# Kernel optimization log

Measured on AMD Instinct MI355X. Metric: run time of the kernel, lower is better.

## Reference

```python
import jax, jax.numpy as jnp
import numpy as np

NEG_SLOPE = 0.01  # torch nn.LeakyReLU default


def setup_inputs() -> dict:
    key = jax.random.key(0)
    k1, k2, k3, k4 = jax.random.split(key, 4)
    N, D = 8192, 64
    x = jax.random.normal(k1, (N, D), dtype=jnp.float32)
    W = jax.random.normal(k2, (D, D), dtype=jnp.float32) * (1.0 / np.sqrt(D))
    b = jax.random.normal(k3, (D,), dtype=jnp.float32) * 0.01
    a = jax.random.normal(k4, (2 * D, 1), dtype=jnp.float32)
    return {"x": x, "W": W, "b": b, "a": a}


def reference(x, W, b, a):
    # h = Linear(x): torch stores weight as [out, in], y = x @ W.T + b
    h = x @ W.T + b  # [N, D]
    D = h.shape[1]
    a1 = a[:D, 0]   # weights on the column node (e_x[i,j] = x_j)
    a2 = a[D:, 0]   # weights on the row node    (e_y[i,j] = x_i)
    s1 = h @ a1     # [N], contribution of node j
    s2 = h @ a2     # [N], contribution of node i
    # score[i, j] = a1.h_j + a2.h_i  (equivalent to expand+concat+matmul)
    scores = s2[:, None] + s1[None, :]                       # [N, N]
    scores = jnp.where(scores >= 0, scores, NEG_SLOPE * scores)  # leaky_relu
    att = jax.nn.softmax(scores, axis=1)                     # softmax over j
    # NOTE: forward multiplies attention with the ORIGINAL x, not h
    return att @ x                                           # [N, D]
```

## Files before the change

kernel.cpp:

```cpp
#include <hip/hip_runtime.h>

#define NEG_SLOPE 0.01f
#define LOG2E 1.4426950408889634f

constexpr int N = 8192;
constexpr int D = 64;
constexpr int PB = 32;
constexpr int RB = 32;
constexpr int NW = 8;

typedef __bf16 bf16x8 __attribute__((ext_vector_type(8)));
typedef float f32x4 __attribute__((ext_vector_type(4)));

#if __has_builtin(__builtin_amdgcn_exp2f)
#define EXP2(x) __builtin_amdgcn_exp2f(x)
#else
#define EXP2(x) exp2f(x)
#endif

__global__ __launch_bounds__(256) void gat_prep(
    const float* __restrict__ x, const float* __restrict__ W_,
    const float* __restrict__ b, const float* __restrict__ a,
    float* __restrict__ s1g, float* __restrict__ s2g,
    float* __restrict__ blockmax, bf16x8* __restrict__ xf) {
  __shared__ float w1s[D], w2s[D], cs[2];
  __shared__ float s1loc[PB];

  const int t = threadIdx.x;
  const int bid = blockIdx.x;

  if (t < 128) {
    const int sel = t >> 6, d = t & 63;
    const float* av = a + sel * D;
    float acc = 0.f;
#pragma unroll
    for (int k = 0; k < D; ++k) acc += W_[k * D + d] * av[k];
    (sel ? w2s : w1s)[d] = acc * LOG2E;
  }
  if (t == 128 || t == 129) {
    const int sel = t - 128;
    float acc = 0.f;
    for (int d = 0; d < D; ++d) acc += b[d] * a[sel * D + d];
    cs[sel] = acc * LOG2E;
  }
  __syncthreads();

  {
    const int r = t >> 3, seg = t & 7;
    const int gi = bid * PB + r;
    const float4 xa = *(const float4*)(x + (size_t)gi * D + seg * 8);
    const float4 xb = *(const float4*)(x + (size_t)gi * D + seg * 8 + 4);
    float p1 = xa.x * w1s[seg * 8 + 0] + xa.y * w1s[seg * 8 + 1] +
               xa.z * w1s[seg * 8 + 2] + xa.w * w1s[seg * 8 + 3] +
               xb.x * w1s[seg * 8 + 4] + xb.y * w1s[seg * 8 + 5] +
               xb.z * w1s[seg * 8 + 6] + xb.w * w1s[seg * 8 + 7];
    float p2 = xa.x * w2s[seg * 8 + 0] + xa.y * w2s[seg * 8 + 1] +
               xa.z * w2s[seg * 8 + 2] + xa.w * w2s[seg * 8 + 3] +
               xb.x * w2s[seg * 8 + 4] + xb.y * w2s[seg * 8 + 5] +
               xb.z * w2s[seg * 8 + 6] + xb.w * w2s[seg * 8 + 7];
#pragma unroll
    for (int off = 4; off; off >>= 1) {
      p1 += __shfl_xor(p1, off, 64);
      p2 += __shfl_xor(p2, off, 64);
    }
    if (seg == 0) {
      const float v1 = p1 + cs[0], v2 = p2 + cs[1];
      s1g[gi] = v1;
      s2g[gi] = v2;
      s1loc[r] = v1;
    }
  }

  {
    const int dt = t >> 6, fl = t & 63;
    const int jb = bid * PB + ((fl >> 4) << 3);
    const int col = dt * 16 + (fl & 15);
    bf16x8 f;
#pragma unroll
    for (int q = 0; q < 8; ++q) f[q] = (__bf16)x[(size_t)(jb + q) * D + col];
    xf[(bid << 8) | (dt << 6) | fl] = f;
  }
  __syncthreads();
  if (t == 0) {
    float m = s1loc[0];
#pragma unroll
    for (int r = 1; r < PB; ++r) m = fmaxf(m, s1loc[r]);
    blockmax[bid] = m;
  }
}

__global__ __launch_bounds__(512, 2) void gat_main(
    const bf16x8* __restrict__ xf, const float* __restrict__ s1g,
    const float* __restrict__ s2g, const float* __restrict__ blockmax,
    float* __restrict__ out) {
  __shared__ float s1s[N];
  __shared__ float accT[NW][RB][65];
  __shared__ float zt[NW][RB];
  __shared__ float gms;

  const int t = threadIdx.x;
  const int lane = t & 63;
  const int w = t >> 6;
  const int arow = lane & 15;
  const int grp = lane >> 4;
  const int ibase = blockIdx.x * RB;

#pragma unroll
  for (int k = 0; k < N / 4 / 512; ++k)
    ((float4*)s1s)[k * 512 + t] = ((const float4*)s1g)[k * 512 + t];

  if (t < 64) {
    float v = fmaxf(fmaxf(blockmax[lane], blockmax[lane + 64]),
                    fmaxf(blockmax[lane + 128], blockmax[lane + 192]));
#pragma unroll
    for (int off = 32; off; off >>= 1) v = fmaxf(v, __shfl_xor(v, off, 64));
    if (lane == 0) gms = v;
  }
  __syncthreads();
  const float gm = gms;

  const float s2v0 = s2g[ibase + arow];
  const float s2v1 = s2g[ibase + 16 + arow];
  const float tm0 = s2v0 + gm, tm1 = s2v1 + gm;
  const float mneg0 = -fmaxf(tm0, NEG_SLOPE * tm0);
  const float mneg1 = -fmaxf(tm1, NEG_SLOPE * tm1);
  const float A0 = s2v0 + mneg0, B0 = fmaf(NEG_SLOPE, s2v0, mneg0);
  const float A1 = s2v1 + mneg1, B1 = fmaf(NEG_SLOPE, s2v1, mneg1);

  f32x4 a00 = {0.f, 0.f, 0.f, 0.f}, a01 = a00, a02 = a00, a03 = a00;
  f32x4 a10 = a00, a11 = a00, a12 = a00, a13 = a00;
  f32x4 az0 = a00, az1 = a00;
  bf16x8 ones;
#pragma unroll
  for (int q = 0; q < 8; ++q) ones[q] = (__bf16)1.0f;

  bf16x8 pA0, pA1, pA2, pA3, pB0, pB1, pB2, pB3;
  {
    const int fa = w << 8;
    pA0 = xf[fa + 0 * 64 + lane]; pA1 = xf[fa + 1 * 64 + lane];
    pA2 = xf[fa + 2 * 64 + lane]; pA3 = xf[fa + 3 * 64 + lane];
    const int fb = (w + NW) << 8;
    pB0 = xf[fb + 0 * 64 + lane]; pB1 = xf[fb + 1 * 64 + lane];
    pB2 = xf[fb + 2 * 64 + lane]; pB3 = xf[fb + 3 * 64 + lane];
  }

  auto process = [&](const bf16x8& x0, const bf16x8& x1, const bf16x8& x2,
                     const bf16x8& x3, int c) {
    const float4 sa = *(const float4*)&s1s[c * 32 + grp * 8];
    const float4 sb = *(const float4*)&s1s[c * 32 + grp * 8 + 4];
    bf16x8 pa0, pa1;
    const float* sv = &sa.x;
#pragma unroll
    for (int q = 0; q < 4; ++q) {
      const float s = sv[q];
      pa0[q] = (__bf16)EXP2(fmaxf(s + A0, fmaf(NEG_SLOPE, s, B0)));
      pa1[q] = (__bf16)EXP2(fmaxf(s + A1, fmaf(NEG_SLOPE, s, B1)));
    }
    const float* sw = &sb.x;
#pragma unroll
    for (int q = 0; q < 4; ++q) {
      const float s = sw[q];
      pa0[4 + q] = (__bf16)EXP2(fmaxf(s + A0, fmaf(NEG_SLOPE, s, B0)));
      pa1[4 + q] = (__bf16)EXP2(fmaxf(s + A1, fmaf(NEG_SLOPE, s, B1)));
    }
    a00 = __builtin_amdgcn_mfma_f32_16x16x32_bf16(pa0, x0, a00, 0, 0, 0);
    a01 = __builtin_amdgcn_mfma_f32_16x16x32_bf16(pa0, x1, a01, 0, 0, 0);
    a02 = __builtin_amdgcn_mfma_f32_16x16x32_bf16(pa0, x2, a02, 0, 0, 0);
    a03 = __builtin_amdgcn_mfma_f32_16x16x32_bf16(pa0, x3, a03, 0, 0, 0);
    az0 = __builtin_amdgcn_mfma_f32_16x16x32_bf16(pa0, ones, az0, 0, 0, 0);
    a10 = __builtin_amdgcn_mfma_f32_16x16x32_bf16(pa1, x0, a10, 0, 0, 0);
    a11 = __builtin_amdgcn_mfma_f32_16x16x32_bf16(pa1, x1, a11, 0, 0, 0);
    a12 = __builtin_amdgcn_mfma_f32_16x16x32_bf16(pa1, x2, a12, 0, 0, 0);
    a13 = __builtin_amdgcn_mfma_f32_16x16x32_bf16(pa1, x3, a13, 0, 0, 0);
    az1 = __builtin_amdgcn_mfma_f32_16x16x32_bf16(pa1, ones, az1, 0, 0, 0);
  };

  int c0 = w;
  constexpr int PAIRS = N / 32 / NW / 2;
  for (int i = 0; i < PAIRS; ++i) {
    process(pA0, pA1, pA2, pA3, c0);
    {
      const int cn = (i == PAIRS - 1) ? c0 : c0 + 2 * NW;
      const int f = cn << 8;
      pA0 = xf[f + 0 * 64 + lane]; pA1 = xf[f + 1 * 64 + lane];
      pA2 = xf[f + 2 * 64 + lane]; pA3 = xf[f + 3 * 64 + lane];
    }
    process(pB0, pB1, pB2, pB3, c0 + NW);
    {
      const int cn = (i == PAIRS - 1) ? c0 + NW : c0 + 3 * NW;
      const int f = cn << 8;
      pB0 = xf[f + 0 * 64 + lane]; pB1 = xf[f + 1 * 64 + lane];
      pB2 = xf[f + 2 * 64 + lane]; pB3 = xf[f + 3 * 64 + lane];
    }
    c0 += 2 * NW;
  }

  if (arow == 0) {
#pragma unroll
    for (int reg = 0; reg < 4; ++reg) {
      zt[w][grp * 4 + reg] = az0[reg];
      zt[w][16 + grp * 4 + reg] = az1[reg];
    }
  }
#pragma unroll
  for (int reg = 0; reg < 4; ++reg) {
    accT[w][grp * 4 + reg][0 * 16 + arow] = a00[reg];
    accT[w][grp * 4 + reg][1 * 16 + arow] = a01[reg];
    accT[w][grp * 4 + reg][2 * 16 + arow] = a02[reg];
    accT[w][grp * 4 + reg][3 * 16 + arow] = a03[reg];
    accT[w][16 + grp * 4 + reg][0 * 16 + arow] = a10[reg];
    accT[w][16 + grp * 4 + reg][1 * 16 + arow] = a11[reg];
    accT[w][16 + grp * 4 + reg][2 * 16 + arow] = a12[reg];
    accT[w][16 + grp * 4 + reg][3 * 16 + arow] = a13[reg];
  }
  __syncthreads();

#pragma unroll
  for (int k = 0; k < 4; ++k) {
    const int r = w * 4 + k;
    float s = 0.f, z = 0.f;
#pragma unroll
    for (int v = 0; v < NW; ++v) {
      s += accT[v][r][lane];
      z += zt[v][r];
    }
    out[(size_t)(ibase + r) * D + lane] = s / z;
  }
}

extern "C" void kernel_launch(void* const* d_in, const int* in_sizes, int n_in,
                              void* d_out, int out_size, void* d_ws, size_t ws_size,
                              hipStream_t stream) {
  const float* x = (const float*)d_in[0];
  const float* W = (const float*)d_in[1];
  const float* b = (const float*)d_in[2];
  const float* a = (const float*)d_in[3];

  float* s1 = (float*)d_ws;
  float* s2 = s1 + N;
  float* blockmax = s2 + N;
  bf16x8* xf = (bf16x8*)((char*)d_ws + (1u << 20));
  float* out = (float*)d_out;

  gat_prep<<<N / PB, 256, 0, stream>>>(x, W, b, a, s1, s2, blockmax, xf);
  gat_main<<<N / RB, 512, 0, stream>>>(xf, s1, s2, blockmax, out);
}
```

Baseline: 83.75 us.

## Double row tile per block and split the key range into two halves

Each block now handles 64 query rows instead of 32, so every loaded xf fragment feeds twice as many MFMAs. The key dimension is split across two blocks per row tile to keep the block count at 256. The partial numerators and denominators are written to workspace and merged by a new combine kernel. This costs more accumulator registers, an extra kernel launch, and a round trip through global memory for the partial outputs.

Result: no change. 83.29 us (-0.6%).

```diff
diff --git a/kernel.cpp b/kernel.cpp
--- a/kernel.cpp
+++ b/kernel.cpp
@@ -6,8 +6,9 @@
 constexpr int N = 8192;
 constexpr int D = 64;
 constexpr int PB = 32;
-constexpr int RB = 32;
+constexpr int RB = 64;
 constexpr int NW = 8;
+constexpr int NWIN_H = 128;
 
 typedef __bf16 bf16x8 __attribute__((ext_vector_type(8)));
 typedef float f32x4 __attribute__((ext_vector_type(4)));
@@ -92,9 +93,9 @@
 __global__ __launch_bounds__(512, 2) void gat_main(
     const bf16x8* __restrict__ xf, const float* __restrict__ s1g,
     const float* __restrict__ s2g, const float* __restrict__ blockmax,
-    float* __restrict__ out) {
-  __shared__ float s1s[N];
-  __shared__ float accT[NW][RB][65];
+    float* __restrict__ pOut, float* __restrict__ pZ) {
+  __shared__ float s1s[NWIN_H * 32];
+  __shared__ float accT[NW][32][65];
   __shared__ float zt[NW][RB];
   __shared__ float gms;
 
@@ -103,11 +104,14 @@
   const int w = t >> 6;
   const int arow = lane & 15;
   const int grp = lane >> 4;
-  const int ibase = blockIdx.x * RB;
-
-#pragma unroll
-  for (int k = 0; k < N / 4 / 512; ++k)
-    ((float4*)s1s)[k * 512 + t] = ((const float4*)s1g)[k * 512 + t];
+  const int bid = blockIdx.x;
+  const int itile = bid >> 1, half = bid & 1;
+  const int ibase = itile * RB;
+  const int jw0 = half * NWIN_H;
+
+#pragma unroll
+  for (int k = 0; k < 2; ++k)
+    ((float4*)s1s)[k * 512 + t] = ((const float4*)(s1g + jw0 * 32))[k * 512 + t];
 
   if (t < 64) {
     float v = fmaxf(fmaxf(blockmax[lane], blockmax[lane + 64]),
@@ -119,49 +123,64 @@
   __syncthreads();
   const float gm = gms;
 
-  const float s2v0 = s2g[ibase + arow];
-  const float s2v1 = s2g[ibase + 16 + arow];
-  const float tm0 = s2v0 + gm, tm1 = s2v1 + gm;
-  const float mneg0 = -fmaxf(tm0, NEG_SLOPE * tm0);
-  const float mneg1 = -fmaxf(tm1, NEG_SLOPE * tm1);
-  const float A0 = s2v0 + mneg0, B0 = fmaf(NEG_SLOPE, s2v0, mneg0);
-  const float A1 = s2v1 + mneg1, B1 = fmaf(NEG_SLOPE, s2v1, mneg1);
+  float A0v, A1v, A2v, A3v, B0v, B1v, B2v, B3v;
+  {
+    const float s0 = s2g[ibase + 0 * 16 + arow];
+    const float s1v = s2g[ibase + 1 * 16 + arow];
+    const float s2v = s2g[ibase + 2 * 16 + arow];
+    const float s3v = s2g[ibase + 3 * 16 + arow];
+    const float t0 = s0 + gm, t1 = s1v + gm, t2 = s2v + gm, t3 = s3v + gm;
+    const float m0 = -fmaxf(t0, NEG_SLOPE * t0);
+    const float m1 = -fmaxf(t1, NEG_SLOPE * t1);
+    const float m2 = -fmaxf(t2, NEG_SLOPE * t2);
+    const float m3 = -fmaxf(t3, NEG_SLOPE * t3);
+    A0v = s0 + m0;  B0v = fmaf(NEG_SLOPE, s0, m0);
+    A1v = s1v + m1; B1v = fmaf(NEG_SLOPE, s1v, m1);
+    A2v = s2v + m2; B2v = fmaf(NEG_SLOPE, s2v, m2);
+    A3v = s3v + m3; B3v = fmaf(NEG_SLOPE, s3v, m3);
+  }
 
   f32x4 a00 = {0.f, 0.f, 0.f, 0.f}, a01 = a00, a02 = a00, a03 = a00;
   f32x4 a10 = a00, a11 = a00, a12 = a00, a13 = a00;
-  f32x4 az0 = a00, az1 = a00;
+  f32x4 a20 = a00, a21 = a00, a22 = a00, a23 = a00;
+  f32x4 a30 = a00, a31 = a00, a32 = a00, a33 = a00;
+  f32x4 az0 = a00, az1 = a00, az2 = a00, az3 = a00;
   bf16x8 ones;
 #pragma unroll
   for (int q = 0; q < 8; ++q) ones[q] = (__bf16)1.0f;
 
-  bf16x8 pA0, pA1, pA2, pA3, pB0, pB1, pB2, pB3;
+  bf16x8 bA0, bA1, bA2, bA3, bB0, bB1, bB2, bB3;
   {
-    const int fa = w << 8;
-    pA0 = xf[fa + 0 * 64 + lane]; pA1 = xf[fa + 1 * 64 + lane];
-    pA2 = xf[fa + 2 * 64 + lane]; pA3 = xf[fa + 3 * 64 + lane];
-    const int fb = (w + NW) << 8;
-    pB0 = xf[fb + 0 * 64 + lane]; pB1 = xf[fb + 1 * 64 + lane];
-    pB2 = xf[fb + 2 * 64 + lane]; pB3 = xf[fb + 3 * 64 + lane];
+    const int fa = (jw0 + w) << 8;
+    bA0 = xf[fa + 0 * 64 + lane]; bA1 = xf[fa + 1 * 64 + lane];
+    bA2 = xf[fa + 2 * 64 + lane]; bA3 = xf[fa + 3 * 64 + lane];
+    const int fb = (jw0 + w + 8) << 8;
+    bB0 = xf[fb + 0 * 64 + lane]; bB1 = xf[fb + 1 * 64 + lane];
+    bB2 = xf[fb + 2 * 64 + lane]; bB3 = xf[fb + 3 * 64 + lane];
   }
 
   auto process = [&](const bf16x8& x0, const bf16x8& x1, const bf16x8& x2,
-                     const bf16x8& x3, int c) {
-    const float4 sa = *(const float4*)&s1s[c * 32 + grp * 8];
-    const float4 sb = *(const float4*)&s1s[c * 32 + grp * 8 + 4];
-    bf16x8 pa0, pa1;
+                     const bf16x8& x3, int lw) {
+    const float4 sa = *(const float4*)&s1s[lw * 32 + grp * 8];
+    const float4 sb = *(const float4*)&s1s[lw * 32 + grp * 8 + 4];
+    bf16x8 pa0, pa1, pa2, pa3;
     const float* sv = &sa.x;
 #pragma unroll
     for (int q = 0; q < 4; ++q) {
       const float s = sv[q];
-      pa0[q] = (__bf16)EXP2(fmaxf(s + A0, fmaf(NEG_SLOPE, s, B0)));
-      pa1[q] = (__bf16)EXP2(fmaxf(s + A1, fmaf(NEG_SLOPE, s, B1)));
+      pa0[q] = (__bf16)EXP2(fmaxf(s + A0v, fmaf(NEG_SLOPE, s, B0v)));
+      pa1[q] = (__bf16)EXP2(fmaxf(s + A1v, fmaf(NEG_SLOPE, s, B1v)));
+      pa2[q] = (__bf16)EXP2(fmaxf(s + A2v, fmaf(NEG_SLOPE, s, B2v)));
+      pa3[q] = (__bf16)EXP2(fmaxf(s + A3v, fmaf(NEG_SLOPE, s, B3v)));
     }
     const float* sw = &sb.x;
 #pragma unroll
     for (int q = 0; q < 4; ++q) {
       const float s = sw[q];
-      pa0[4 + q] = (__bf16)EXP2(fmaxf(s + A0, fmaf(NEG_SLOPE, s, B0)));
-      pa1[4 + q] = (__bf16)EXP2(fmaxf(s + A1, fmaf(NEG_SLOPE, s, B1)));
+      pa0[4 + q] = (__bf16)EXP2(fmaxf(s + A0v, fmaf(NEG_SLOPE, s, B0v)));
+      pa1[4 + q] = (__bf16)EXP2(fmaxf(s + A1v, fmaf(NEG_SLOPE, s, B1v)));
+      pa2[4 + q] = (__bf16)EXP2(fmaxf(s + A2v, fmaf(NEG_SLOPE, s, B2v)));
+      pa3[4 + q] = (__bf16)EXP2(fmaxf(s + A3v, fmaf(NEG_SLOPE, s, B3v)));
     }
     a00 = __builtin_amdgcn_mfma_f32_16x16x32_bf16(pa0, x0, a00, 0, 0, 0);
     a01 = __builtin_amdgcn_mfma_f32_16x16x32_bf16(pa0, x1, a01, 0, 0, 0);
@@ -173,58 +192,110 @@
     a12 = __builtin_amdgcn_mfma_f32_16x16x32_bf16(pa1, x2, a12, 0, 0, 0);
     a13 = __builtin_amdgcn_mfma_f32_16x16x32_bf16(pa1, x3, a13, 0, 0, 0);
     az1 = __builtin_amdgcn_mfma_f32_16x16x32_bf16(pa1, ones, az1, 0, 0, 0);
+    a20 = __builtin_amdgcn_mfma_f32_16x16x32_bf16(pa2, x0, a20, 0, 0, 0);
+    a21 = __builtin_amdgcn_mfma_f32_16x16x32_bf16(pa2, x1, a21, 0, 0, 0);
+    a22 = __builtin_amdgcn_mfma_f32_16x16x32_bf16(pa2, x2, a22, 0, 0, 0);
+    a23 = __builtin_amdgcn_mfma_f32_16x16x32_bf16(pa2, x3, a23, 0, 0, 0);
+    az2 = __builtin_amdgcn_mfma_f32_16x16x32_bf16(pa2, ones, az2, 0, 0, 0);
+    a30 = __builtin_amdgcn_mfma_f32_16x16x32_bf16(pa3, x0, a30, 0, 0, 0);
+    a31 = __builtin_amdgcn_mfma_f32_16x16x32_bf16(pa3, x1, a31, 0, 0, 0);
+    a32 = __builtin_amdgcn_mfma_f32_16x16x32_bf16(pa3, x2, a32, 0, 0, 0);
+    a33 = __builtin_amdgcn_mfma_f32_16x16x32_bf16(pa3, x3, a33, 0, 0, 0);
+    az3 = __builtin_amdgcn_mfma_f32_16x16x32_bf16(pa3, ones, az3, 0, 0, 0);
   };
 
-  int c0 = w;
-  constexpr int PAIRS = N / 32 / NW / 2;
-  for (int i = 0; i < PAIRS; ++i) {
-    process(pA0, pA1, pA2, pA3, c0);
+  for (int it = 0; it < 8; ++it) {
+    const int lwA = w + 16 * it;
+    process(bA0, bA1, bA2, bA3, lwA);
     {
-      const int cn = (i == PAIRS - 1) ? c0 : c0 + 2 * NW;
-      const int f = cn << 8;
-      pA0 = xf[f + 0 * 64 + lane]; pA1 = xf[f + 1 * 64 + lane];
-      pA2 = xf[f + 2 * 64 + lane]; pA3 = xf[f + 3 * 64 + lane];
-    }
-    process(pB0, pB1, pB2, pB3, c0 + NW);
+      const int lwn = (it == 7) ? lwA : lwA + 16;
+      const int f = (jw0 + lwn) << 8;
+      bA0 = xf[f + 0 * 64 + lane]; bA1 = xf[f + 1 * 64 + lane];
+      bA2 = xf[f + 2 * 64 + lane]; bA3 = xf[f + 3 * 64 + lane];
+    }
+    const int lwB = w + 16 * it + 8;
+    process(bB0, bB1, bB2, bB3, lwB);
     {
-      const int cn = (i == PAIRS - 1) ? c0 + NW : c0 + 3 * NW;
-      const int f = cn << 8;
-      pB0 = xf[f + 0 * 64 + lane]; pB1 = xf[f + 1 * 64 + lane];
-      pB2 = xf[f + 2 * 64 + lane]; pB3 = xf[f + 3 * 64 + lane];
-    }
-    c0 += 2 * NW;
+      const int lwn = (it == 7) ? lwB : lwB + 16;
+      const int f = (jw0 + lwn) << 8;
+      bB0 = xf[f + 0 * 64 + lane]; bB1 = xf[f + 1 * 64 + lane];
+      bB2 = xf[f + 2 * 64 + lane]; bB3 = xf[f + 3 * 64 + lane];
+    }
   }
 
   if (arow == 0) {
 #pragma unroll
     for (int reg = 0; reg < 4; ++reg) {
-      zt[w][grp * 4 + reg] = az0[reg];
-      zt[w][16 + grp * 4 + reg] = az1[reg];
-    }
-  }
-#pragma unroll
-  for (int reg = 0; reg < 4; ++reg) {
-    accT[w][grp * 4 + reg][0 * 16 + arow] = a00[reg];
-    accT[w][grp * 4 + reg][1 * 16 + arow] = a01[reg];
-    accT[w][grp * 4 + reg][2 * 16 + arow] = a02[reg];
-    accT[w][grp * 4 + reg][3 * 16 + arow] = a03[reg];
-    accT[w][16 + grp * 4 + reg][0 * 16 + arow] = a10[reg];
-    accT[w][16 + grp * 4 + reg][1 * 16 + arow] = a11[reg];
-    accT[w][16 + grp * 4 + reg][2 * 16 + arow] = a12[reg];
-    accT[w][16 + grp * 4 + reg][3 * 16 + arow] = a13[reg];
-  }
-  __syncthreads();
-
-#pragma unroll
-  for (int k = 0; k < 4; ++k) {
-    const int r = w * 4 + k;
-    float s = 0.f, z = 0.f;
-#pragma unroll
-    for (int v = 0; v < NW; ++v) {
-      s += accT[v][r][lane];
-      z += zt[v][r];
-    }
-    out[(size_t)(ibase + r) * D + lane] = s / z;
+      zt[w][0 * 16 + grp * 4 + reg] = az0[reg];
+      zt[w][1 * 16 + grp * 4 + reg] = az1[reg];
+      zt[w][2 * 16 + grp * 4 + reg] = az2[reg];
+      zt[w][3 * 16 + grp * 4 + reg] = az3[reg];
+    }
+  }
+
+#pragma unroll
+  for (int h = 0; h < 2; ++h) {
+    if (h) __syncthreads();
+#pragma unroll
+    for (int reg = 0; reg < 4; ++reg) {
+      if (h == 0) {
+        accT[w][0 * 16 + grp * 4 + reg][0 * 16 + arow] = a00[reg];
+        accT[w][0 * 16 + grp * 4 + reg][1 * 16 + arow] = a01[reg];
+        accT[w][0 * 16 + grp * 4 + reg][2 * 16 + arow] = a02[reg];
+        accT[w][0 * 16 + grp * 4 + reg][3 * 16 + arow] = a03[reg];
+        accT[w][1 * 16 + grp * 4 + reg][0 * 16 + arow] = a10[reg];
+        accT[w][1 * 16 + grp * 4 + reg][1 * 16 + arow] = a11[reg];
+        accT[w][1 * 16 + grp * 4 + reg][2 * 16 + arow] = a12[reg];
+        accT[w][1 * 16 + grp * 4 + reg][3 * 16 + arow] = a13[reg];
+      } else {
+        accT[w][0 * 16 + grp * 4 + reg][0 * 16 + arow] = a20[reg];
+        accT[w][0 * 16 + grp * 4 + reg][1 * 16 + arow] = a21[reg];
+        accT[w][0 * 16 + grp * 4 + reg][2 * 16 + arow] = a22[reg];
+        accT[w][0 * 16 + grp * 4 + reg][3 * 16 + arow] = a23[reg];
+        accT[w][1 * 16 + grp * 4 + reg][0 * 16 + arow] = a30[reg];
+        accT[w][1 * 16 + grp * 4 + reg][1 * 16 + arow] = a31[reg];
+        accT[w][1 * 16 + grp * 4 + reg][2 * 16 + arow] = a32[reg];
+        accT[w][1 * 16 + grp * 4 + reg][3 * 16 + arow] = a33[reg];
+      }
+    }
+    __syncthreads();
+#pragma unroll
+    for (int k = 0; k < 4; ++k) {
+      const int rloc = w * 4 + k;
+      float s = 0.f;
+#pragma unroll
+      for (int v = 0; v < NW; ++v) s += accT[v][rloc][lane];
+      const int grow = ibase + h * 32 + rloc;
+      pOut[((size_t)half * N + grow) * D + lane] = s;
+    }
+  }
+
+  if (t < RB) {
+    float z = 0.f;
+#pragma unroll
+    for (int v = 0; v < NW; ++v) z += zt[v][t];
+    pZ[half * N + ibase + t] = z;
+  }
+}
+
+__global__ __launch_bounds__(256) void gat_comb(
+    const float* __restrict__ pOut, const float* __restrict__ pZ,
+    float* __restrict__ out) {
+  const int t = threadIdx.x;
+  const int base = blockIdx.x * 512 + t;
+#pragma unroll
+  for (int k = 0; k < 2; ++k) {
+    const int f4 = base + k * 256;
+    const int row = f4 >> 4;
+    const float inv = 1.0f / (pZ[row] + pZ[N + row]);
+    const float4 p0 = ((const float4*)pOut)[f4];
+    const float4 p1 = ((const float4*)pOut)[(N * D / 4) + f4];
+    float4 o;
+    o.x = (p0.x + p1.x) * inv;
+    o.y = (p0.y + p1.y) * inv;
+    o.z = (p0.z + p1.z) * inv;
+    o.w = (p0.w + p1.w) * inv;
+    ((float4*)out)[f4] = o;
   }
 }
 
@@ -236,12 +307,16 @@
   const float* b = (const float*)d_in[2];
   const float* a = (const float*)d_in[3];
 
-  float* s1 = (float*)d_ws;
+  float* ws = (float*)d_ws;
+  float* s1 = ws;
   float* s2 = s1 + N;
   float* blockmax = s2 + N;
   bf16x8* xf = (bf16x8*)((char*)d_ws + (1u << 20));
+  float* pOut = (float*)((char*)d_ws + (4u << 20));
+  float* pZ = (float*)((char*)d_ws + (8u << 20));
   float* out = (float*)d_out;
 
   gat_prep<<<N / PB, 256, 0, stream>>>(x, W, b, a, s1, s2, blockmax, xf);
-  gat_main<<<N / RB, 512, 0, stream>>>(xf, s1, s2, blockmax, out);
+  gat_main<<<(N / RB) * 2, 512, 0, stream>>>(xf, s1, s2, blockmax, pOut, pZ);
+  gat_comb<<<256, 256, 0, stream>>>(pOut, pZ, out);
 }
```
